# Kernel tuning notes

Measured on AMD Instinct MI355X. Metric: run time of the kernel, lower is better.

## Reference

```python
import jax, jax.numpy as jnp
import numpy as np

N_NODES = 50000
N_EDGES = 800000
N_RELS = 65
D = 64
N_GRAPHS = 512


def setup_inputs() -> dict:
    key = jax.random.key(0)
    ks = jax.random.split(key, 20)
    inp = {
        "node_feats": jax.random.normal(ks[0], (N_NODES, D), dtype=jnp.float32),
        "etypes": jax.random.randint(ks[1], (N_EDGES,), 0, N_RELS),
        "src": jax.random.randint(ks[2], (N_EDGES,), 0, N_NODES),
        "dst": jax.random.randint(ks[3], (N_EDGES,), 0, N_NODES),
        "graph_ids": jnp.sort(jax.random.randint(ks[4], (N_NODES,), 0, N_GRAPHS)),
    }
    s = 1.0 / np.sqrt(D)
    # 3 RGCN layers: per-relation weights (basis with num_bases=num_rels == full) + bias
    for i, k in zip(range(1, 4), (ks[5], ks[6], ks[7])):
        inp[f"W_rel{i}"] = jax.random.normal(k, (N_RELS, D, D), dtype=jnp.float32) * s
        inp[f"b{i}"] = jnp.zeros((D,), dtype=jnp.float32)
    # 3 FC layers
    for i, k in zip(range(1, 4), (ks[8], ks[9], ks[10])):
        inp[f"fc_W{i}"] = jax.random.normal(k, (D, D), dtype=jnp.float32) * s
        inp[f"fc_b{i}"] = jnp.zeros((D,), dtype=jnp.float32)
    inp["pred_W"] = jax.random.normal(ks[11], (D, 2), dtype=jnp.float32) * s
    inp["pred_b"] = jnp.zeros((2,), dtype=jnp.float32)
    return inp


def _rgcn_layer(h, W, b, etypes, src, dst):
    # all-relation projection: [N, R, K]
    proj = jnp.einsum('nd,rdk->nrk', h, W)
    # per-edge gather of relation-specific message: [E, K]
    msg = proj[src, etypes]
    # scatter-sum into destination nodes
    agg = jax.ops.segment_sum(msg, dst, num_segments=h.shape[0])
    return jax.nn.relu(agg + b)


def reference(node_feats, etypes, src, dst, graph_ids,
              W_rel1, b1, W_rel2, b2, W_rel3, b3,
              fc_W1, fc_b1, fc_W2, fc_b2, fc_W3, fc_b3,
              pred_W, pred_b):
    h = node_feats
    h = _rgcn_layer(h, W_rel1, b1, etypes, src, dst)
    h = _rgcn_layer(h, W_rel2, b2, etypes, src, dst)
    h = _rgcn_layer(h, W_rel3, b3, etypes, src, dst)
    # sum-pool nodes per graph: [G, D]
    g = jax.ops.segment_sum(h, graph_ids, num_segments=N_GRAPHS)
    g = jax.nn.relu(g @ fc_W1 + fc_b1)
    g = jax.nn.relu(g @ fc_W2 + fc_b2)
    g = jax.nn.relu(g @ fc_W3 + fc_b3)
    return g @ pred_W + pred_b
```

## Files before the change

### kernel.cpp

```cpp
#include <hip/hip_runtime.h>
#include <hip/hip_bf16.h>

#define N_NODES 50000
#define N_EDGES 800000
#define N_RELS 65
#define DIM 64
#define N_GRAPHS 512

#define SORT_BLOCKS 1024
#define CHUNK ((N_EDGES + SORT_BLOCKS - 1) / SORT_BLOCKS)

#define SCAN_BLK 512
#define NSCAN_BLKS ((N_NODES + SCAN_BLK - 1) / SCAN_BLK)

#define MSG_BLOCKS 2048
#define NWAVES (MSG_BLOCKS * 4)

typedef __attribute__((ext_vector_type(8))) short short8;
typedef __attribute__((ext_vector_type(4))) float f32x4;


__global__ void conv_h_zero_kernel(const float* __restrict__ x, __hip_bfloat16* __restrict__ y,
                                   int* __restrict__ cnt_d, int* __restrict__ cnt_g) {
    int i = blockIdx.x * 256 + threadIdx.x;
    if (i < (N_NODES * DIM) / 4) {
        float4 v = *(const float4*)(x + (size_t)i * 4);
        unsigned short us[4];
        us[0] = __hip_bfloat16_raw(__float2bfloat16(v.x)).x;
        us[1] = __hip_bfloat16_raw(__float2bfloat16(v.y)).x;
        us[2] = __hip_bfloat16_raw(__float2bfloat16(v.z)).x;
        us[3] = __hip_bfloat16_raw(__float2bfloat16(v.w)).x;
        *(ushort4*)(y + (size_t)i * 4) = *(const ushort4*)us;
    }
    if (i < N_NODES) cnt_d[i] = 0;
    if (i < N_GRAPHS) cnt_g[i] = 0;
}


__global__ __launch_bounds__(256) void wconv_kernel(
    const float* __restrict__ W1, const float* __restrict__ W2,
    const float* __restrict__ W3,
    __hip_bfloat16* __restrict__ Wt1, __hip_bfloat16* __restrict__ Wt2,
    __hip_bfloat16* __restrict__ Wt3) {
    __shared__ float tile[64][65];
    int b = blockIdx.x;
    int which = b / N_RELS, r = b - which * N_RELS;
    const float* W = (which == 0) ? W1 : (which == 1) ? W2 : W3;
    __hip_bfloat16* Wt = (which == 0) ? Wt1 : (which == 1) ? Wt2 : Wt3;
    int t = threadIdx.x;
    for (int i = t; i < 4096; i += 256) {
        int row = i >> 6, col = i & 63;
        tile[row][col] = W[(size_t)r * 4096 + i];
    }
    __syncthreads();
    for (int i = t; i < 4096; i += 256) {
        int row = i >> 6, col = i & 63;
        Wt[(size_t)r * 4096 + i] = __float2bfloat16(tile[col][row]);
    }
}


__global__ __launch_bounds__(256) void hist_all_kernel(
    const int* __restrict__ et, const int* __restrict__ gid,
    int* __restrict__ blk_hist, int* __restrict__ cnt_g) {
    __shared__ int lh[N_RELS];
    int t = threadIdx.x, b = blockIdx.x;
    int gtid = b * 256 + t;
    if (t < N_RELS) lh[t] = 0;
    __syncthreads();
    int lo = b * CHUNK;
    int hi = lo + CHUNK; if (hi > N_EDGES) hi = N_EDGES;
    for (int i = lo + t; i < hi; i += 256)
        atomicAdd(&lh[et[i]], 1);
    for (int i = gtid; i < N_NODES; i += SORT_BLOCKS * 256)
        atomicAdd(&cnt_g[gid[i]], 1);
    __syncthreads();
    if (t < N_RELS) blk_hist[t * SORT_BLOCKS + b] = lh[t];
}


__global__ __launch_bounds__(256) void relscan_kernel(const int* __restrict__ blk_hist,
                                                      int* __restrict__ blk_off,
                                                      int* __restrict__ rel_tot) {
    __shared__ int wsum[4];
    int r = blockIdx.x;
    int t = threadIdx.x;
    int w = t >> 6, lane = t & 63;
    const int PER = SORT_BLOCKS / 256;
    int4 v0 = *(const int4*)(blk_hist + (size_t)r * SORT_BLOCKS + t * PER);
    int vals[4] = {v0.x, v0.y, v0.z, v0.w};
    int s = 0;
    #pragma unroll
    for (int j = 0; j < PER; ++j) s += vals[j];
    int x = s;
    #pragma unroll
    for (int off = 1; off < 64; off <<= 1) {
        int y = __shfl_up(x, off);
        if (lane >= off) x += y;
    }
    if (lane == 63) wsum[w] = x;
    __syncthreads();
    int base = 0;
    for (int i = 0; i < w; ++i) base += wsum[i];
    int run = base + x - s;
    int out[4];
    #pragma unroll
    for (int j = 0; j < PER; ++j) { out[j] = run; run += vals[j]; }
    *(int4*)(blk_off + (size_t)r * SORT_BLOCKS + t * PER) = *(const int4*)&out[0];
    if (t == 255) rel_tot[r] = base + x;
}


__global__ __launch_bounds__(64) void reltop_kernel(const int* __restrict__ rel_tot,
                                                    int* __restrict__ rel_ptr,
                                                    int* __restrict__ tile_base) {
    if (threadIdx.x == 0) {
        int s = 0, tt = 0;
        for (int q = 0; q < N_RELS; ++q) {
            int v = rel_tot[q];
            rel_ptr[q] = s; s += v;
            tile_base[q] = tt; tt += (v + 15) >> 4;
        }
        rel_ptr[N_RELS] = N_EDGES;
        tile_base[N_RELS] = tt;
    }
}


__global__ __launch_bounds__(256) void scatter2_kernel(
    const int* __restrict__ et, const int* __restrict__ src,
    const int* __restrict__ dst, const int* __restrict__ blk_hist,
    const int* __restrict__ blk_off, const int* __restrict__ rel_ptr,
    unsigned long long* __restrict__ epk, int* __restrict__ cnt_d) {
    __shared__ unsigned long long buf[CHUNK];
    __shared__ unsigned char relof[CHUNK];
    __shared__ int loff[N_RELS + 1];
    __shared__ int lcur[N_RELS];
    __shared__ int gbase[N_RELS];
    int t = threadIdx.x, b = blockIdx.x;

    if (t < 64) {
        int v = blk_hist[t * SORT_BLOCKS + b];
        int x = v;
        #pragma unroll
        for (int off = 1; off < 64; off <<= 1) {
            int y = __shfl_up(x, off);
            if (t >= off) x += y;
        }
        loff[t] = x - v;
        lcur[t] = x - v;
        gbase[t] = rel_ptr[t] + blk_off[t * SORT_BLOCKS + b];
        if (t == 63) { loff[64] = x; lcur[64] = x; }
    } else if (t == 64) {
        gbase[64] = rel_ptr[64] + blk_off[64 * SORT_BLOCKS + b];
    }
    __syncthreads();

    int lo = b * CHUNK;
    int hi = lo + CHUNK; if (hi > N_EDGES) hi = N_EDGES;
    int nloc = hi - lo;

    #pragma unroll
    for (int k = 0; k < 4; ++k) {
        int i = lo + t + k * 256;
        if (i < hi) {
            int r = et[i], d = dst[i];
            unsigned s = (unsigned)src[i];
            int rank = atomicAdd(&cnt_d[d], 1);
            int pl = atomicAdd(&lcur[r], 1);
            unsigned lo32 = s | ((unsigned)d << 16);
            buf[pl] = (unsigned long long)lo32 |
                      ((unsigned long long)(unsigned)rank << 32);
            relof[pl] = (unsigned char)r;
        }
    }
    __syncthreads();

    #pragma unroll
    for (int k = 0; k < 4; ++k) {
        int i = t + k * 256;
        if (i < nloc) {
            int r = relof[i];
            epk[gbase[r] + i - loff[r]] = buf[i];
        }
    }
}


__global__ __launch_bounds__(SCAN_BLK) void scanblk_kernel(const int* __restrict__ cnt,
                                                           int* __restrict__ outv,
                                                           int* __restrict__ blk_tot) {
    __shared__ int tmp[SCAN_BLK];
    int t = threadIdx.x;
    int i = blockIdx.x * SCAN_BLK + t;
    int v = (i < N_NODES) ? cnt[i] : 0;
    tmp[t] = v;
    __syncthreads();
    for (int off = 1; off < SCAN_BLK; off <<= 1) {
        int add = (t >= off) ? tmp[t - off] : 0;
        __syncthreads();
        tmp[t] += add;
        __syncthreads();
    }
    if (i < N_NODES) outv[i] = tmp[t] - v;
    if (t == SCAN_BLK - 1) blk_tot[blockIdx.x] = tmp[t];
}

__global__ __launch_bounds__(64) void scantop_gid_kernel(
    const int* __restrict__ blk_tot, int* __restrict__ blk_base,
    const int* __restrict__ cnt_g, int* __restrict__ g_ptr) {
    int lane = threadIdx.x;
    if (blockIdx.x == 0) {
        if (lane == 0) {
            int run = 0;
            for (int b = 0; b < NSCAN_BLKS; ++b) { blk_base[b] = run; run += blk_tot[b]; }
        }
    } else {
        int run = 0;
        for (int c = 0; c < N_GRAPHS; c += 64) {
            int v = cnt_g[c + lane];
            int x = v;
            #pragma unroll
            for (int off = 1; off < 64; off <<= 1) {
                int y = __shfl_up(x, off);
                if (lane >= off) x += y;
            }
            g_ptr[c + lane] = run + x - v;
            run += __shfl(x, 63);
        }
    }
}

__global__ __launch_bounds__(SCAN_BLK) void scanadd_kernel(int* __restrict__ outv,
                                                           const int* __restrict__ blk_base) {
    int i = blockIdx.x * SCAN_BLK + threadIdx.x;
    if (i < N_NODES) outv[i] += blk_base[blockIdx.x];
}

__global__ void unpack_kernel(const unsigned long long* __restrict__ epk,
                              const int* __restrict__ row_ptr,
                              int* __restrict__ src_s, int* __restrict__ dpos) {
    int i = blockIdx.x * 256 + threadIdx.x;
    if (i < N_EDGES) {
        unsigned long long e = epk[i];
        int s = (int)(e & 0xFFFFu);
        int d = (int)((e >> 16) & 0xFFFFu);
        int rank = (int)(e >> 32);
        src_s[i] = s;
        dpos[i] = rank + row_ptr[d];
    }
}


__device__ inline unsigned pack2bf(float x, float y) {
    unsigned short ux = __hip_bfloat16_raw(__float2bfloat16(x)).x;
    unsigned short uy = __hip_bfloat16_raw(__float2bfloat16(y)).x;
    return (unsigned)ux | ((unsigned)uy << 16);
}

__global__ __launch_bounds__(256) void msg_mfma_kernel(
    const __hip_bfloat16* __restrict__ hb, const __hip_bfloat16* __restrict__ Wt,
    const int* __restrict__ rel_ptr, const int* __restrict__ tile_base,
    const int* __restrict__ src_s, const int* __restrict__ dpos,
    __hip_bfloat16* __restrict__ msg) {
    int t = threadIdx.x;
    int w = t >> 6, lane = t & 63;
    int quad = lane >> 4, m16 = lane & 15;
    int wave = blockIdx.x * 4 + w;

    int ntiles = tile_base[N_RELS];
    int tpw = (ntiles + NWAVES - 1) / NWAVES;
    int T = wave * tpw;
    int T1 = T + tpw; if (T1 > ntiles) T1 = ntiles;
    if (T >= T1) return;

    int r = 0;
    while (T >= tile_base[r + 1]) ++r;

    while (T < T1) {
        int chunk_end = tile_base[r + 1]; if (chunk_end > T1) chunk_end = T1;
        int e_base = rel_ptr[r], t_base = tile_base[r];
        int seg_end = rel_ptr[r + 1];

        const __hip_bfloat16* Wr = Wt + (size_t)r * (DIM * DIM);
        short8 bf00 = *(const short8*)(Wr + (4 * m16)     * DIM + quad * 8);
        short8 bf01 = *(const short8*)(Wr + (4 * m16 + 1) * DIM + quad * 8);
        short8 bf02 = *(const short8*)(Wr + (4 * m16 + 2) * DIM + quad * 8);
        short8 bf03 = *(const short8*)(Wr + (4 * m16 + 3) * DIM + quad * 8);
        short8 bf10 = *(const short8*)(Wr + (4 * m16)     * DIM + 32 + quad * 8);
        short8 bf11 = *(const short8*)(Wr + (4 * m16 + 1) * DIM + 32 + quad * 8);
        short8 bf12 = *(const short8*)(Wr + (4 * m16 + 2) * DIM + 32 + quad * 8);
        short8 bf13 = *(const short8*)(Wr + (4 * m16 + 3) * DIM + 32 + quad * 8);

        auto loadidx = [&](int TT, int& sv, int& dp) {
            int TC = TT < chunk_end ? TT : chunk_end - 1;
            int i = e_base + (TC - t_base) * 16 + lane;
            if (i >= N_EDGES) i = N_EDGES - 1;
            sv = src_s[i]; dp = dpos[i];
        };
        auto gatherA = [&](int sv, short8& x0, short8& x1) {
            int s = __shfl(sv, m16);
            const __hip_bfloat16* hp = hb + (size_t)s * DIM + quad * 8;
            x0 = *(const short8*)hp;
            x1 = *(const short8*)(hp + 32);
        };

        int sv0, dp0, sv1, dp1, sv2, dp2;
        short8 a0c, a1c, a0n, a1n;
        loadidx(T,     sv0, dp0);
        loadidx(T + 1, sv1, dp1);
        gatherA(sv0, a0c, a1c);

        for (; T < chunk_end; ++T) {
            loadidx(T + 2, sv2, dp2);
            gatherA(sv1, a0n, a1n);

            int e0 = e_base + (T - t_base) * 16;
            int rows = seg_end - e0; if (rows > 16) rows = 16;

            f32x4 c0 = {0.f, 0.f, 0.f, 0.f}, c1 = c0, c2 = c0, c3 = c0;
            c0 = __builtin_amdgcn_mfma_f32_16x16x32_bf16(a0c, bf00, c0, 0, 0, 0);
            c1 = __builtin_amdgcn_mfma_f32_16x16x32_bf16(a0c, bf01, c1, 0, 0, 0);
            c2 = __builtin_amdgcn_mfma_f32_16x16x32_bf16(a0c, bf02, c2, 0, 0, 0);
            c3 = __builtin_amdgcn_mfma_f32_16x16x32_bf16(a0c, bf03, c3, 0, 0, 0);
            c0 = __builtin_amdgcn_mfma_f32_16x16x32_bf16(a1c, bf10, c0, 0, 0, 0);
            c1 = __builtin_amdgcn_mfma_f32_16x16x32_bf16(a1c, bf11, c1, 0, 0, 0);
            c2 = __builtin_amdgcn_mfma_f32_16x16x32_bf16(a1c, bf12, c2, 0, 0, 0);
            c3 = __builtin_amdgcn_mfma_f32_16x16x32_bf16(a1c, bf13, c3, 0, 0, 0);

            int dpr[4];
            #pragma unroll
            for (int g = 0; g < 4; ++g) dpr[g] = __shfl(dp0, quad * 4 + g);

            #pragma unroll
            for (int g = 0; g < 4; ++g) {
                if (quad * 4 + g < rows) {
                    uint2 pk;
                    pk.x = pack2bf(c0[g], c1[g]);
                    pk.y = pack2bf(c2[g], c3[g]);
                    *(uint2*)(msg + (size_t)dpr[g] * DIM + 4 * m16) = pk;
                }
            }

            sv0 = sv1; dp0 = dp1; sv1 = sv2; dp1 = dp2;
            a0c = a0n; a1c = a1n;
        }
        ++r;
        while (T < T1 && T >= tile_base[r + 1]) ++r;
    }
}


__global__ __launch_bounds__(256) void agg_kernel(
    const __hip_bfloat16* __restrict__ msg, const int* __restrict__ row_ptr,
    const int* __restrict__ cnt_d, const float* __restrict__ b,
    __hip_bfloat16* __restrict__ hout) {
    int wave = blockIdx.x * 4 + (threadIdx.x >> 6);
    int lane = threadIdx.x & 63;
    if (wave >= N_NODES) return;
    int j0 = row_ptr[wave];
    int n  = cnt_d[wave];
    int rgrp = lane >> 3, dgrp = lane & 7;

    float a[8] = {0.f, 0.f, 0.f, 0.f, 0.f, 0.f, 0.f, 0.f};
    for (int jj = 0; jj < n; jj += 8) {
        int row = jj + rgrp;
        if (row < n) {
            uint4 d = *(const uint4*)(msg + (size_t)(j0 + row) * DIM + dgrp * 8);
            a[0] += __uint_as_float(d.x << 16);
            a[1] += __uint_as_float(d.x & 0xffff0000u);
            a[2] += __uint_as_float(d.y << 16);
            a[3] += __uint_as_float(d.y & 0xffff0000u);
            a[4] += __uint_as_float(d.z << 16);
            a[5] += __uint_as_float(d.z & 0xffff0000u);
            a[6] += __uint_as_float(d.w << 16);
            a[7] += __uint_as_float(d.w & 0xffff0000u);
        }
    }
    #pragma unroll
    for (int i = 0; i < 8; ++i) {
        a[i] += __shfl_xor(a[i], 8);
        a[i] += __shfl_xor(a[i], 16);
        a[i] += __shfl_xor(a[i], 32);
    }
    if (rgrp == 0) {
        unsigned short us[8];
        #pragma unroll
        for (int i = 0; i < 8; ++i) {
            float v = a[i] + b[dgrp * 8 + i];
            us[i] = __hip_bfloat16_raw(__float2bfloat16(v > 0.f ? v : 0.f)).x;
        }
        *(uint4*)(hout + (size_t)wave * DIM + dgrp * 8) = *(const uint4*)us;
    }
}


__global__ __launch_bounds__(256) void poolfc_kernel(
    const __hip_bfloat16* __restrict__ h, const int* __restrict__ g_ptr,
    const int* __restrict__ cnt_g,
    const float* __restrict__ W1, const float* __restrict__ b1,
    const float* __restrict__ W2, const float* __restrict__ b2,
    const float* __restrict__ W3, const float* __restrict__ b3,
    const float* __restrict__ pW, const float* __restrict__ pb,
    float* __restrict__ out) {
    int wave = blockIdx.x * 4 + (threadIdx.x >> 6);
    int lane = threadIdx.x & 63;
    if (wave >= N_GRAPHS) return;
    int j0 = g_ptr[wave];
    int n  = cnt_g[wave];
    int rgrp = lane >> 3, dgrp = lane & 7;

    float a[8] = {0.f, 0.f, 0.f, 0.f, 0.f, 0.f, 0.f, 0.f};
    for (int jj = 0; jj < n; jj += 8) {
        int row = jj + rgrp;
        if (row < n) {
            uint4 d = *(const uint4*)(h + (size_t)(j0 + row) * DIM + dgrp * 8);
            a[0] += __uint_as_float(d.x << 16);
            a[1] += __uint_as_float(d.x & 0xffff0000u);
            a[2] += __uint_as_float(d.y << 16);
            a[3] += __uint_as_float(d.y & 0xffff0000u);
            a[4] += __uint_as_float(d.z << 16);
            a[5] += __uint_as_float(d.z & 0xffff0000u);
            a[6] += __uint_as_float(d.w << 16);
            a[7] += __uint_as_float(d.w & 0xffff0000u);
        }
    }
    #pragma unroll
    for (int i = 0; i < 8; ++i) {
        a[i] += __shfl_xor(a[i], 8);
        a[i] += __shfl_xor(a[i], 16);
        a[i] += __shfl_xor(a[i], 32);
    }
    float v;
    {
        float acc = b1[lane];
        #pragma unroll
        for (int o = 0; o < 8; ++o)
            #pragma unroll
            for (int q = 0; q < 8; ++q)
                acc += __shfl(a[o], q) * W1[(q * 8 + o) * DIM + lane];
        v = acc > 0.f ? acc : 0.f;
    }
    {
        float acc = b2[lane];
        #pragma unroll
        for (int d = 0; d < DIM; ++d)
            acc += __shfl(v, d) * W2[d * DIM + lane];
        v = acc > 0.f ? acc : 0.f;
    }
    {
        float acc = b3[lane];
        #pragma unroll
        for (int d = 0; d < DIM; ++d)
            acc += __shfl(v, d) * W3[d * DIM + lane];
        v = acc > 0.f ? acc : 0.f;
    }
    float p0 = v * pW[lane * 2 + 0];
    float p1 = v * pW[lane * 2 + 1];
    #pragma unroll
    for (int off = 32; off > 0; off >>= 1) {
        p0 += __shfl_down(p0, off);
        p1 += __shfl_down(p1, off);
    }
    if (lane == 0) {
        out[wave * 2 + 0] = p0 + pb[0];
        out[wave * 2 + 1] = p1 + pb[1];
    }
}


extern "C" void kernel_launch(void* const* d_in, const int* in_sizes, int n_in,
                              void* d_out, int out_size, void* d_ws, size_t ws_size,
                              hipStream_t stream) {
    const float* node_feats = (const float*)d_in[0];
    const int*   etypes     = (const int*)d_in[1];
    const int*   src        = (const int*)d_in[2];
    const int*   dst        = (const int*)d_in[3];
    const int*   graph_ids  = (const int*)d_in[4];
    const float* W1 = (const float*)d_in[5];
    const float* b1 = (const float*)d_in[6];
    const float* W2 = (const float*)d_in[7];
    const float* b2 = (const float*)d_in[8];
    const float* W3 = (const float*)d_in[9];
    const float* b3 = (const float*)d_in[10];
    const float* fcW1 = (const float*)d_in[11];
    const float* fcb1 = (const float*)d_in[12];
    const float* fcW2 = (const float*)d_in[13];
    const float* fcb2 = (const float*)d_in[14];
    const float* fcW3 = (const float*)d_in[15];
    const float* fcb3 = (const float*)d_in[16];
    const float* pW = (const float*)d_in[17];
    const float* pb = (const float*)d_in[18];
    float* out = (float*)d_out;

    char* p = (char*)d_ws;
    auto alloc = [&](size_t bytes) -> void* {
        void* r = (void*)p;
        p += (bytes + 255) & ~(size_t)255;
        return r;
    };
    int* blk_hist  = (int*)alloc((size_t)SORT_BLOCKS * N_RELS * sizeof(int));
    int* blk_off   = (int*)alloc((size_t)SORT_BLOCKS * N_RELS * sizeof(int));
    int* rel_ptr   = (int*)alloc((N_RELS + 1) * sizeof(int));
    int* rel_tot   = (int*)alloc(N_RELS * sizeof(int));
    int* tile_base = (int*)alloc((N_RELS + 1) * sizeof(int));
    unsigned long long* epk = (unsigned long long*)alloc((size_t)N_EDGES * sizeof(unsigned long long));
    int* src_s     = (int*)alloc((size_t)N_EDGES * sizeof(int));
    int* dpos      = (int*)alloc((size_t)N_EDGES * sizeof(int));
    int* cnt_d     = (int*)alloc((size_t)N_NODES * sizeof(int));
    int* row_ptr   = (int*)alloc((size_t)N_NODES * sizeof(int));
    int* blk_tot   = (int*)alloc(NSCAN_BLKS * sizeof(int));
    int* blk_base  = (int*)alloc(NSCAN_BLKS * sizeof(int));
    int* cnt_g     = (int*)alloc(N_GRAPHS * sizeof(int));
    int* g_ptr     = (int*)alloc(N_GRAPHS * sizeof(int));
    __hip_bfloat16* hb0 = (__hip_bfloat16*)alloc((size_t)N_NODES * DIM * sizeof(__hip_bfloat16));
    __hip_bfloat16* hb1 = (__hip_bfloat16*)alloc((size_t)N_NODES * DIM * sizeof(__hip_bfloat16));
    __hip_bfloat16* Wt1 = (__hip_bfloat16*)alloc((size_t)N_RELS * DIM * DIM * sizeof(__hip_bfloat16));
    __hip_bfloat16* Wt2 = (__hip_bfloat16*)alloc((size_t)N_RELS * DIM * DIM * sizeof(__hip_bfloat16));
    __hip_bfloat16* Wt3 = (__hip_bfloat16*)alloc((size_t)N_RELS * DIM * DIM * sizeof(__hip_bfloat16));
    __hip_bfloat16* msg = (__hip_bfloat16*)alloc((size_t)N_EDGES * DIM * sizeof(__hip_bfloat16));

    const int EBLK = (N_EDGES + 255) / 256;
    const int CBLK = (N_NODES * DIM / 4 + 255) / 256;
    const int AGG_BLOCKS = (N_NODES + 3) / 4;

    conv_h_zero_kernel<<<CBLK, 256, 0, stream>>>(node_feats, hb0, cnt_d, cnt_g);
    wconv_kernel<<<3 * N_RELS, 256, 0, stream>>>(W1, W2, W3, Wt1, Wt2, Wt3);
    hist_all_kernel<<<SORT_BLOCKS, 256, 0, stream>>>(etypes, graph_ids, blk_hist, cnt_g);
    relscan_kernel<<<N_RELS, 256, 0, stream>>>(blk_hist, blk_off, rel_tot);
    reltop_kernel<<<1, 64, 0, stream>>>(rel_tot, rel_ptr, tile_base);
    scatter2_kernel<<<SORT_BLOCKS, 256, 0, stream>>>(etypes, src, dst, blk_hist, blk_off,
                                                     rel_ptr, epk, cnt_d);
    scanblk_kernel<<<NSCAN_BLKS, SCAN_BLK, 0, stream>>>(cnt_d, row_ptr, blk_tot);
    scantop_gid_kernel<<<2, 64, 0, stream>>>(blk_tot, blk_base, cnt_g, g_ptr);
    scanadd_kernel<<<NSCAN_BLKS, SCAN_BLK, 0, stream>>>(row_ptr, blk_base);
    unpack_kernel<<<EBLK, 256, 0, stream>>>(epk, row_ptr, src_s, dpos);

    msg_mfma_kernel<<<MSG_BLOCKS, 256, 0, stream>>>(hb0, Wt1, rel_ptr, tile_base,
                                                    src_s, dpos, msg);
    agg_kernel<<<AGG_BLOCKS, 256, 0, stream>>>(msg, row_ptr, cnt_d, b1, hb1);

    msg_mfma_kernel<<<MSG_BLOCKS, 256, 0, stream>>>(hb1, Wt2, rel_ptr, tile_base,
                                                    src_s, dpos, msg);
    agg_kernel<<<AGG_BLOCKS, 256, 0, stream>>>(msg, row_ptr, cnt_d, b2, hb0);

    msg_mfma_kernel<<<MSG_BLOCKS, 256, 0, stream>>>(hb0, Wt3, rel_ptr, tile_base,
                                                    src_s, dpos, msg);
    agg_kernel<<<AGG_BLOCKS, 256, 0, stream>>>(msg, row_ptr, cnt_d, b3, hb1);

    poolfc_kernel<<<(N_GRAPHS + 3) / 4, 256, 0, stream>>>(hb1, g_ptr, cnt_g,
                                                          fcW1, fcb1, fcW2, fcb2,
                                                          fcW3, fcb3, pW, pb, out);
}
```

Baseline: 383.4 us.

## Fuse preprocessing kernels and replace small scan kernels with last-block tickets

Merges bf16 conversion, weight transposition and the relation histogram into one prep kernel. The tiny top-level scan kernels are folded into their producers using an atomic last-block ticket. The scan-add pass is dropped: consumers add the block base on the fly, and graph offsets come from binary search on the sorted graph ids instead of atomic counting. This cuts launch count and serial gaps in the preprocessing chain, at the cost of an extra load per lookup in the aggregation and unpack kernels and reliance on the threadfence-plus-ticket ordering.

After: 366.0 us. 4.5% less time.

```diff
diff --git a/kernel.cpp b/kernel.cpp
--- a/kernel.cpp
+++ b/kernel.cpp
@@ -20,10 +20,31 @@
 typedef __attribute__((ext_vector_type(4))) float f32x4;
 
 
-__global__ void conv_h_zero_kernel(const float* __restrict__ x, __hip_bfloat16* __restrict__ y,
-                                   int* __restrict__ cnt_d, int* __restrict__ cnt_g) {
-    int i = blockIdx.x * 256 + threadIdx.x;
-    if (i < (N_NODES * DIM) / 4) {
+__global__ __launch_bounds__(256) void prep_kernel(
+    const float* __restrict__ x, const int* __restrict__ et,
+    __hip_bfloat16* __restrict__ y, int* __restrict__ cnt_d,
+    int* __restrict__ blk_hist,
+    const float* __restrict__ W1, const float* __restrict__ W2,
+    const float* __restrict__ W3,
+    __hip_bfloat16* __restrict__ Wt1, __hip_bfloat16* __restrict__ Wt2,
+    __hip_bfloat16* __restrict__ Wt3,
+    int* __restrict__ done_flags) {
+    __shared__ int lh[N_RELS];
+    __shared__ float tile[64][65];
+    int t = threadIdx.x, b = blockIdx.x;
+    int gtid = b * 256 + t;
+
+    if (gtid < N_NODES) cnt_d[gtid] = 0;
+    if (gtid < 2) done_flags[gtid] = 0;
+
+    if (t < N_RELS) lh[t] = 0;
+    __syncthreads();
+    int lo = b * CHUNK;
+    int hi = lo + CHUNK; if (hi > N_EDGES) hi = N_EDGES;
+    for (int i = lo + t; i < hi; i += 256)
+        atomicAdd(&lh[et[i]], 1);
+
+    for (int i = gtid; i < (N_NODES * DIM) / 4; i += SORT_BLOCKS * 256) {
         float4 v = *(const float4*)(x + (size_t)i * 4);
         unsigned short us[4];
         us[0] = __hip_bfloat16_raw(__float2bfloat16(v.x)).x;
@@ -32,48 +53,22 @@
         us[3] = __hip_bfloat16_raw(__float2bfloat16(v.w)).x;
         *(ushort4*)(y + (size_t)i * 4) = *(const ushort4*)us;
     }
-    if (i < N_NODES) cnt_d[i] = 0;
-    if (i < N_GRAPHS) cnt_g[i] = 0;
-}
-
-
-__global__ __launch_bounds__(256) void wconv_kernel(
-    const float* __restrict__ W1, const float* __restrict__ W2,
-    const float* __restrict__ W3,
-    __hip_bfloat16* __restrict__ Wt1, __hip_bfloat16* __restrict__ Wt2,
-    __hip_bfloat16* __restrict__ Wt3) {
-    __shared__ float tile[64][65];
-    int b = blockIdx.x;
-    int which = b / N_RELS, r = b - which * N_RELS;
-    const float* W = (which == 0) ? W1 : (which == 1) ? W2 : W3;
-    __hip_bfloat16* Wt = (which == 0) ? Wt1 : (which == 1) ? Wt2 : Wt3;
-    int t = threadIdx.x;
-    for (int i = t; i < 4096; i += 256) {
-        int row = i >> 6, col = i & 63;
-        tile[row][col] = W[(size_t)r * 4096 + i];
-    }
-    __syncthreads();
-    for (int i = t; i < 4096; i += 256) {
-        int row = i >> 6, col = i & 63;
-        Wt[(size_t)r * 4096 + i] = __float2bfloat16(tile[col][row]);
-    }
-}
-
-
-__global__ __launch_bounds__(256) void hist_all_kernel(
-    const int* __restrict__ et, const int* __restrict__ gid,
-    int* __restrict__ blk_hist, int* __restrict__ cnt_g) {
-    __shared__ int lh[N_RELS];
-    int t = threadIdx.x, b = blockIdx.x;
-    int gtid = b * 256 + t;
-    if (t < N_RELS) lh[t] = 0;
-    __syncthreads();
-    int lo = b * CHUNK;
-    int hi = lo + CHUNK; if (hi > N_EDGES) hi = N_EDGES;
-    for (int i = lo + t; i < hi; i += 256)
-        atomicAdd(&lh[et[i]], 1);
-    for (int i = gtid; i < N_NODES; i += SORT_BLOCKS * 256)
-        atomicAdd(&cnt_g[gid[i]], 1);
+
+    if (b < 3 * N_RELS) {
+        int which = b / N_RELS, r = b - which * N_RELS;
+        const float* W = (which == 0) ? W1 : (which == 1) ? W2 : W3;
+        __hip_bfloat16* Wt = (which == 0) ? Wt1 : (which == 1) ? Wt2 : Wt3;
+        for (int i = t; i < 4096; i += 256) {
+            int row = i >> 6, col = i & 63;
+            tile[row][col] = W[(size_t)r * 4096 + i];
+        }
+        __syncthreads();
+        for (int i = t; i < 4096; i += 256) {
+            int row = i >> 6, col = i & 63;
+            Wt[(size_t)r * 4096 + i] = __float2bfloat16(tile[col][row]);
+        }
+    }
+
     __syncthreads();
     if (t < N_RELS) blk_hist[t * SORT_BLOCKS + b] = lh[t];
 }
@@ -81,7 +76,10 @@
 
 __global__ __launch_bounds__(256) void relscan_kernel(const int* __restrict__ blk_hist,
                                                       int* __restrict__ blk_off,
-                                                      int* __restrict__ rel_tot) {
+                                                      int* __restrict__ rel_tot,
+                                                      int* __restrict__ rel_ptr,
+                                                      int* __restrict__ tile_base,
+                                                      int* __restrict__ done) {
     __shared__ int wsum[4];
     int r = blockIdx.x;
     int t = threadIdx.x;
@@ -107,22 +105,22 @@
     #pragma unroll
     for (int j = 0; j < PER; ++j) { out[j] = run; run += vals[j]; }
     *(int4*)(blk_off + (size_t)r * SORT_BLOCKS + t * PER) = *(const int4*)&out[0];
-    if (t == 255) rel_tot[r] = base + x;
-}
-
-
-__global__ __launch_bounds__(64) void reltop_kernel(const int* __restrict__ rel_tot,
-                                                    int* __restrict__ rel_ptr,
-                                                    int* __restrict__ tile_base) {
-    if (threadIdx.x == 0) {
-        int s = 0, tt = 0;
-        for (int q = 0; q < N_RELS; ++q) {
-            int v = rel_tot[q];
-            rel_ptr[q] = s; s += v;
-            tile_base[q] = tt; tt += (v + 15) >> 4;
-        }
-        rel_ptr[N_RELS] = N_EDGES;
-        tile_base[N_RELS] = tt;
+
+    if (t == 255) {
+        __hip_atomic_store(&rel_tot[r], base + x, __ATOMIC_RELAXED, __HIP_MEMORY_SCOPE_AGENT);
+        __threadfence();
+        int ticket = atomicAdd(done, 1);
+        if (ticket == N_RELS - 1) {
+            int ss = 0, tt = 0;
+            for (int q = 0; q < N_RELS; ++q) {
+                int v = __hip_atomic_load(&rel_tot[q], __ATOMIC_RELAXED,
+                                          __HIP_MEMORY_SCOPE_AGENT);
+                rel_ptr[q] = ss; ss += v;
+                tile_base[q] = tt; tt += (v + 15) >> 4;
+            }
+            rel_ptr[N_RELS] = N_EDGES;
+            tile_base[N_RELS] = tt;
+        }
     }
 }
 
@@ -187,10 +185,13 @@
 }
 
 
-__global__ __launch_bounds__(SCAN_BLK) void scanblk_kernel(const int* __restrict__ cnt,
-                                                           int* __restrict__ outv,
-                                                           int* __restrict__ blk_tot) {
+__global__ __launch_bounds__(SCAN_BLK) void scanblk_kernel(
+    const int* __restrict__ cnt, int* __restrict__ outv,
+    int* __restrict__ blk_tot, int* __restrict__ blk_base,
+    const int* __restrict__ gid, int* __restrict__ g_ptr,
+    int* __restrict__ cnt_g, int* __restrict__ done) {
     __shared__ int tmp[SCAN_BLK];
+    __shared__ int is_last;
     int t = threadIdx.x;
     int i = blockIdx.x * SCAN_BLK + t;
     int v = (i < N_NODES) ? cnt[i] : 0;
@@ -203,42 +204,41 @@
         __syncthreads();
     }
     if (i < N_NODES) outv[i] = tmp[t] - v;
-    if (t == SCAN_BLK - 1) blk_tot[blockIdx.x] = tmp[t];
-}
-
-__global__ __launch_bounds__(64) void scantop_gid_kernel(
-    const int* __restrict__ blk_tot, int* __restrict__ blk_base,
-    const int* __restrict__ cnt_g, int* __restrict__ g_ptr) {
-    int lane = threadIdx.x;
-    if (blockIdx.x == 0) {
-        if (lane == 0) {
+    if (t == SCAN_BLK - 1) {
+        __hip_atomic_store(&blk_tot[blockIdx.x], tmp[t], __ATOMIC_RELAXED,
+                           __HIP_MEMORY_SCOPE_AGENT);
+        __threadfence();
+        int ticket = atomicAdd(done, 1);
+        is_last = (ticket == NSCAN_BLKS - 1) ? 1 : 0;
+    }
+    __syncthreads();
+    if (is_last) {
+        if (t == 0) {
             int run = 0;
-            for (int b = 0; b < NSCAN_BLKS; ++b) { blk_base[b] = run; run += blk_tot[b]; }
-        }
-    } else {
-        int run = 0;
-        for (int c = 0; c < N_GRAPHS; c += 64) {
-            int v = cnt_g[c + lane];
-            int x = v;
-            #pragma unroll
-            for (int off = 1; off < 64; off <<= 1) {
-                int y = __shfl_up(x, off);
-                if (lane >= off) x += y;
+            for (int b2 = 0; b2 < NSCAN_BLKS; ++b2) {
+                int v2 = __hip_atomic_load(&blk_tot[b2], __ATOMIC_RELAXED,
+                                           __HIP_MEMORY_SCOPE_AGENT);
+                blk_base[b2] = run; run += v2;
             }
-            g_ptr[c + lane] = run + x - v;
-            run += __shfl(x, 63);
-        }
-    }
-}
-
-__global__ __launch_bounds__(SCAN_BLK) void scanadd_kernel(int* __restrict__ outv,
-                                                           const int* __restrict__ blk_base) {
-    int i = blockIdx.x * SCAN_BLK + threadIdx.x;
-    if (i < N_NODES) outv[i] += blk_base[blockIdx.x];
-}
+        }
+        if (t < N_GRAPHS) {
+            int g = t;
+            int lo2 = 0, hi2 = N_NODES;
+            while (lo2 < hi2) { int m = (lo2 + hi2) >> 1; if (gid[m] < g) lo2 = m + 1; else hi2 = m; }
+            int a2 = lo2;
+            lo2 = 0; hi2 = N_NODES;
+            int g1 = g + 1;
+            while (lo2 < hi2) { int m = (lo2 + hi2) >> 1; if (gid[m] < g1) lo2 = m + 1; else hi2 = m; }
+            g_ptr[g] = a2;
+            cnt_g[g] = lo2 - a2;
+        }
+    }
+}
+
 
 __global__ void unpack_kernel(const unsigned long long* __restrict__ epk,
-                              const int* __restrict__ row_ptr,
+                              const int* __restrict__ outv,
+                              const int* __restrict__ blk_base,
                               int* __restrict__ src_s, int* __restrict__ dpos) {
     int i = blockIdx.x * 256 + threadIdx.x;
     if (i < N_EDGES) {
@@ -247,7 +247,7 @@
         int d = (int)((e >> 16) & 0xFFFFu);
         int rank = (int)(e >> 32);
         src_s[i] = s;
-        dpos[i] = rank + row_ptr[d];
+        dpos[i] = rank + outv[d] + blk_base[d >> 9];
     }
 }
 
@@ -352,13 +352,14 @@
 
 
 __global__ __launch_bounds__(256) void agg_kernel(
-    const __hip_bfloat16* __restrict__ msg, const int* __restrict__ row_ptr,
+    const __hip_bfloat16* __restrict__ msg, const int* __restrict__ outv,
+    const int* __restrict__ blk_base,
     const int* __restrict__ cnt_d, const float* __restrict__ b,
     __hip_bfloat16* __restrict__ hout) {
     int wave = blockIdx.x * 4 + (threadIdx.x >> 6);
     int lane = threadIdx.x & 63;
     if (wave >= N_NODES) return;
-    int j0 = row_ptr[wave];
+    int j0 = outv[wave] + blk_base[wave >> 9];
     int n  = cnt_d[wave];
     int rgrp = lane >> 3, dgrp = lane & 7;
 
@@ -508,11 +509,12 @@
     int* src_s     = (int*)alloc((size_t)N_EDGES * sizeof(int));
     int* dpos      = (int*)alloc((size_t)N_EDGES * sizeof(int));
     int* cnt_d     = (int*)alloc((size_t)N_NODES * sizeof(int));
-    int* row_ptr   = (int*)alloc((size_t)N_NODES * sizeof(int));
+    int* outv      = (int*)alloc((size_t)N_NODES * sizeof(int));
     int* blk_tot   = (int*)alloc(NSCAN_BLKS * sizeof(int));
     int* blk_base  = (int*)alloc(NSCAN_BLKS * sizeof(int));
     int* cnt_g     = (int*)alloc(N_GRAPHS * sizeof(int));
     int* g_ptr     = (int*)alloc(N_GRAPHS * sizeof(int));
+    int* done_flags= (int*)alloc(2 * sizeof(int));
     __hip_bfloat16* hb0 = (__hip_bfloat16*)alloc((size_t)N_NODES * DIM * sizeof(__hip_bfloat16));
     __hip_bfloat16* hb1 = (__hip_bfloat16*)alloc((size_t)N_NODES * DIM * sizeof(__hip_bfloat16));
     __hip_bfloat16* Wt1 = (__hip_bfloat16*)alloc((size_t)N_RELS * DIM * DIM * sizeof(__hip_bfloat16));
@@ -521,32 +523,30 @@
     __hip_bfloat16* msg = (__hip_bfloat16*)alloc((size_t)N_EDGES * DIM * sizeof(__hip_bfloat16));
 
     const int EBLK = (N_EDGES + 255) / 256;
-    const int CBLK = (N_NODES * DIM / 4 + 255) / 256;
     const int AGG_BLOCKS = (N_NODES + 3) / 4;
 
-    conv_h_zero_kernel<<<CBLK, 256, 0, stream>>>(node_feats, hb0, cnt_d, cnt_g);
-    wconv_kernel<<<3 * N_RELS, 256, 0, stream>>>(W1, W2, W3, Wt1, Wt2, Wt3);
-    hist_all_kernel<<<SORT_BLOCKS, 256, 0, stream>>>(etypes, graph_ids, blk_hist, cnt_g);
-    relscan_kernel<<<N_RELS, 256, 0, stream>>>(blk_hist, blk_off, rel_tot);
-    reltop_kernel<<<1, 64, 0, stream>>>(rel_tot, rel_ptr, tile_base);
+    prep_kernel<<<SORT_BLOCKS, 256, 0, stream>>>(node_feats, etypes, hb0, cnt_d, blk_hist,
+                                                 W1, W2, W3, Wt1, Wt2, Wt3, done_flags);
+    relscan_kernel<<<N_RELS, 256, 0, stream>>>(blk_hist, blk_off, rel_tot,
+                                               rel_ptr, tile_base, &done_flags[0]);
     scatter2_kernel<<<SORT_BLOCKS, 256, 0, stream>>>(etypes, src, dst, blk_hist, blk_off,
                                                      rel_ptr, epk, cnt_d);
-    scanblk_kernel<<<NSCAN_BLKS, SCAN_BLK, 0, stream>>>(cnt_d, row_ptr, blk_tot);
-    scantop_gid_kernel<<<2, 64, 0, stream>>>(blk_tot, blk_base, cnt_g, g_ptr);
-    scanadd_kernel<<<NSCAN_BLKS, SCAN_BLK, 0, stream>>>(row_ptr, blk_base);
-    unpack_kernel<<<EBLK, 256, 0, stream>>>(epk, row_ptr, src_s, dpos);
+    scanblk_kernel<<<NSCAN_BLKS, SCAN_BLK, 0, stream>>>(cnt_d, outv, blk_tot, blk_base,
+                                                        graph_ids, g_ptr, cnt_g,
+                                                        &done_flags[1]);
+    unpack_kernel<<<EBLK, 256, 0, stream>>>(epk, outv, blk_base, src_s, dpos);
 
     msg_mfma_kernel<<<MSG_BLOCKS, 256, 0, stream>>>(hb0, Wt1, rel_ptr, tile_base,
                                                     src_s, dpos, msg);
-    agg_kernel<<<AGG_BLOCKS, 256, 0, stream>>>(msg, row_ptr, cnt_d, b1, hb1);
+    agg_kernel<<<AGG_BLOCKS, 256, 0, stream>>>(msg, outv, blk_base, cnt_d, b1, hb1);
 
     msg_mfma_kernel<<<MSG_BLOCKS, 256, 0, stream>>>(hb1, Wt2, rel_ptr, tile_base,
                                                     src_s, dpos, msg);
-    agg_kernel<<<AGG_BLOCKS, 256, 0, stream>>>(msg, row_ptr, cnt_d, b2, hb0);
+    agg_kernel<<<AGG_BLOCKS, 256, 0, stream>>>(msg, outv, blk_base, cnt_d, b2, hb0);
 
     msg_mfma_kernel<<<MSG_BLOCKS, 256, 0, stream>>>(hb0, Wt3, rel_ptr, tile_base,
                                                     src_s, dpos, msg);
-    agg_kernel<<<AGG_BLOCKS, 256, 0, stream>>>(msg, row_ptr, cnt_d, b3, hb1);
+    agg_kernel<<<AGG_BLOCKS, 256, 0, stream>>>(msg, outv, blk_base, cnt_d, b3, hb1);
 
     poolfc_kernel<<<(N_GRAPHS + 3) / 4, 256, 0, stream>>>(hb1, g_ptr, cnt_g,
                                                           fcW1, fcb1, fcW2, fcb2,
```
